# Kernel tuning notes

Measured on AMD Instinct MI355X. Metric: run time of the kernel, lower is better.

## Reference

```python
import jax, jax.numpy as jnp
import numpy as np

B, L, D, H = 2, 2048, 2048, 16
Dh = D // H
THETA = 500000.0


def _init_rope(dim, seq_len, n_heads):
    # Returns freqs_cis of shape (1, seq_len, 1, head_dim//2, 2) -> [..., 0]=cos, [..., 1]=sin
    hd = dim // n_heads
    inv_freqs = 1.0 / (THETA ** (jnp.arange(0, hd, 2, dtype=jnp.float32) / hd))
    t = jnp.arange(seq_len, dtype=jnp.float32)
    freqs = jnp.outer(t, inv_freqs).astype(jnp.float32)  # (L, hd/2)
    fc = jnp.stack([jnp.cos(freqs)[None, :, None, :],
                    jnp.sin(freqs)[None, :, None, :]], axis=3)  # (1, L, 1, 2, hd/2)
    return fc.transpose(0, 1, 2, 4, 3)  # (1, L, 1, hd/2, 2)


def _apply_rope(q, k, freqs_cis):
    def rotate(x):
        x2 = x.reshape(*x.shape[:-1], -1, 2)  # (B, L, H, Dh/2, 2)
        f = freqs_cis[:, :x.shape[1]]
        cos, sin = f[..., 0], f[..., 1]
        r = jnp.stack([x2[..., 0] * cos - x2[..., 1] * sin,
                       x2[..., 1] * cos + x2[..., 0] * sin], axis=-1)
        return r.reshape(*x.shape)
    return rotate(q), rotate(k)


def setup_inputs() -> dict:
    key = jax.random.key(0)
    kx, kq, kk, kv, ko = jax.random.split(key, 5)
    scale = 1.0 / np.sqrt(D)
    x = jax.random.normal(kx, (B, L, D), dtype=jnp.float32)
    Wq = jax.random.normal(kq, (D, H, Dh), dtype=jnp.float32) * scale
    Wk = jax.random.normal(kk, (D, H, Dh), dtype=jnp.float32) * scale
    Wv = jax.random.normal(kv, (D, H, Dh), dtype=jnp.float32) * scale
    Wo = jax.random.normal(ko, (D, D), dtype=jnp.float32) * scale
    return {"x": x, "Wq": Wq, "Wk": Wk, "Wv": Wv, "Wo": Wo}


def reference(x, Wq, Wk, Wv, Wo):
    freqs_cis = _init_rope(D, L, H)
    q = jnp.einsum('bld,dhk->blhk', x, Wq)  # (B, L, H, Dh)
    k = jnp.einsum('bld,dhk->blhk', x, Wk)
    v = jnp.einsum('bld,dhk->blhk', x, Wv)
    q, k = _apply_rope(q, k, freqs_cis)
    q = q / (Dh ** 0.5)
    att = jnp.einsum('bqhd,bkhd->bhqk', q, k)  # (B, H, L, L)
    Lq = x.shape[1]
    mask = jnp.tril(jnp.ones((1, 1, Lq, Lq), dtype=jnp.bool_))
    neg_inf = jnp.finfo(jnp.float32).min
    att = jnp.where(mask, att, neg_inf)
    att = jax.nn.softmax(att, axis=-1)
    out = jnp.einsum('bhqk,bkhd->bqhd', att, v)  # (B, L, H, Dh)
    out = out.reshape(x.shape)
    return jnp.einsum('bld,de->ble', out, Wo)
```

## Files before the change

### kernel.cpp

```cpp
#include <hip/hip_runtime.h>

typedef unsigned short u16;
typedef unsigned int u32;

#define Bb 2
#define Lc 2048
#define Dc 2048
#define Hc 16
#define DhC 128

typedef __bf16 bf16x8 __attribute__((ext_vector_type(8)));
typedef float f32x4 __attribute__((ext_vector_type(4)));
typedef float f32x16 __attribute__((ext_vector_type(16)));

__device__ __forceinline__ u16 f2b(float f) {
  u32 u = __float_as_uint(f);
  u32 r = (u + 0x7fffu + ((u >> 16) & 1u)) >> 16;
  return (u16)r;
}
__device__ __forceinline__ float b2f(u16 u) {
  return __uint_as_float(((u32)u) << 16);
}

__device__ __forceinline__ u32 cvtpk(float lo, float hi) {
  u32 r;
  asm("v_cvt_pk_bf16_f32 %0, %1, %2" : "=v"(r) : "v"(lo), "v"(hi));
  return r;
}

__device__ __forceinline__ void gll16(const void* g, void* l) {
  __builtin_amdgcn_global_load_lds(
      (const __attribute__((address_space(1))) u32*)g,
      (__attribute__((address_space(3))) u32*)l, 16, 0, 0);
}

__global__ __launch_bounds__(256) void sniff_dtype(const u16* __restrict__ x,
                                                   int* __restrict__ flag) {
  __shared__ int bad;
  if (threadIdx.x == 0) bad = 0;
  __syncthreads();
  int local = 0;
  for (int i = threadIdx.x; i < 65536; i += 256) {
    float v = fabsf(b2f(x[i]));
    if (!(v < 1000.f)) local = 1;
  }
  if (local) atomicOr(&bad, 1);
  __syncthreads();
  if (threadIdx.x == 0) *flag = bad;
}

__global__ __launch_bounds__(256) void conv_x(const void* __restrict__ in,
                                              u16* __restrict__ out,
                                              const int* __restrict__ flag) {
  const int f32 = *flag;
  const int i0 = (blockIdx.x * 256 + threadIdx.x) * 4;
  if (f32) {
    const float* p = (const float*)in;
#pragma unroll
    for (int j = 0; j < 4; j++) out[i0 + j] = f2b(p[i0 + j]);
  } else {
    const u16* p = (const u16*)in;
#pragma unroll
    for (int j = 0; j < 4; j++) out[i0 + j] = p[i0 + j];
  }
}

__device__ __forceinline__ void tconv_body(const void* in, u16* out, int f32) {
  __shared__ __align__(16) u16 tile[64][65];
  const int r0 = blockIdx.y * 64, c0 = blockIdx.x * 64;
  const int tc = threadIdx.x & 63, tr4 = threadIdx.x >> 6;
#pragma unroll
  for (int p = 0; p < 16; p++) {
    int r = tr4 + p * 4;
    size_t idx = (size_t)(r0 + r) * 2048 + c0 + tc;
    tile[r][tc] = f32 ? f2b(((const float*)in)[idx]) : ((const u16*)in)[idx];
  }
  __syncthreads();
#pragma unroll
  for (int p = 0; p < 16; p++) {
    int rr = tr4 + p * 4;
    out[(size_t)(c0 + rr) * 2048 + r0 + tc] = tile[tc][rr];
  }
}

__global__ __launch_bounds__(256) void transpose2d_conv(const void* __restrict__ in,
                                                        u16* __restrict__ out,
                                                        const int* __restrict__ flag) {
  tconv_body(in, out, *flag);
}

__global__ __launch_bounds__(256) void transpose3_conv(const void* __restrict__ W0,
                                                       const void* __restrict__ W1,
                                                       const void* __restrict__ W2,
                                                       u16* __restrict__ out,
                                                       const int* __restrict__ flag) {
  const int z = blockIdx.z;
  const void* in = (z == 0) ? W0 : (z == 1) ? W1 : W2;
  tconv_body(in, out + (size_t)z * 2048 * 2048, *flag);
}

template <typename OutT, int BN, bool FUSEV>
__device__ __forceinline__ void g256f_core(const u16* __restrict__ A,
                                           const u16* __restrict__ Bt,
                                           OutT* __restrict__ C,
                                           u16* __restrict__ Vt,
                                           int nwg, size_t bufStride) {
  constexpr int K = 2048;
  constexpr int WNW = (BN == 256) ? 4 : 2;
  constexpr int MT = (BN == 256) ? 8 : 4;
  constexpr int NT = 4;
  __shared__ __align__(16) u16 Asl[3][256 * 32];
  __shared__ __align__(16) u16 Bsl[3][BN * 32];

  const int tid = threadIdx.x;
  const int lane = tid & 63, w = tid >> 6;
  const int quad = lane >> 4, l15 = lane & 15;
  const int wm = w / WNW, wn = w % WNW;

  const int q8 = nwg >> 3;
  const int id = (int)blockIdx.x;
  const int swz = (id & 7) * q8 + (id >> 3);
  const int m0 = (swz & 15) * 256;
  const int n0 = (swz >> 4) * BN;

  const u16* aS = A + (size_t)(m0 + w * 16 + l15) * K + quad * 8;
  const u16* bS = Bt + (size_t)(n0 + w * 16 + l15) * K + quad * 8;

  const f32x4 fz = {0.f, 0.f, 0.f, 0.f};
  f32x4 acc[MT][NT];
#pragma unroll
  for (int i = 0; i < MT; i++)
#pragma unroll
    for (int j = 0; j < NT; j++) acc[i][j] = fz;

  auto stagef = [&](int kidx, int sl) {
    const int kk = kidx * 32;
    gll16(aS + kk, &Asl[sl][w * 512]);
    gll16(aS + (size_t)128 * K + kk, &Asl[sl][(8 + w) * 512]);
    gll16(bS + kk, &Bsl[sl][w * 512]);
    if constexpr (BN == 256)
      gll16(bS + (size_t)128 * K + kk, &Bsl[sl][(8 + w) * 512]);
  };

  auto computef = [&](int sl) {
    bf16x8 afr[MT], bfr[NT];
#pragma unroll
    for (int nt = 0; nt < NT; nt++)
      bfr[nt] = *(const bf16x8*)(&Bsl[sl][(wn * NT + nt) * 512 + lane * 8]);
#pragma unroll
    for (int mt = 0; mt < MT / 2; mt++)
      afr[mt] = *(const bf16x8*)(&Asl[sl][(wm * MT + mt) * 512 + lane * 8]);
    __builtin_amdgcn_sched_barrier(0);
#pragma unroll
    for (int mt = MT / 2; mt < MT; mt++)
      afr[mt] = *(const bf16x8*)(&Asl[sl][(wm * MT + mt) * 512 + lane * 8]);
    if constexpr (MT == 8)
      asm volatile("s_waitcnt lgkmcnt(4)" ::: "memory");
    else
      asm volatile("s_waitcnt lgkmcnt(2)" ::: "memory");
    __builtin_amdgcn_sched_barrier(0);
    __builtin_amdgcn_s_setprio(1);
#pragma unroll
    for (int mt = 0; mt < MT / 2; mt++)
#pragma unroll
      for (int nt = 0; nt < NT; nt++)
        acc[mt][nt] = __builtin_amdgcn_mfma_f32_16x16x32_bf16(
            afr[mt], bfr[nt], acc[mt][nt], 0, 0, 0);
    asm volatile("s_waitcnt lgkmcnt(0)" ::: "memory");
    __builtin_amdgcn_sched_barrier(0);
#pragma unroll
    for (int mt = MT / 2; mt < MT; mt++)
#pragma unroll
      for (int nt = 0; nt < NT; nt++)
        acc[mt][nt] = __builtin_amdgcn_mfma_f32_16x16x32_bf16(
            afr[mt], bfr[nt], acc[mt][nt], 0, 0, 0);
    __builtin_amdgcn_s_setprio(0);
  };

#define GVW()                                                                \
  do {                                                                       \
    if constexpr (BN == 256)                                                 \
      asm volatile("s_waitcnt vmcnt(4)" ::: "memory");                       \
    else                                                                     \
      asm volatile("s_waitcnt vmcnt(3)" ::: "memory");                       \
  } while (0)

  stagef(0, 0);
  stagef(1, 1);
  GVW();
  __builtin_amdgcn_s_barrier();

  int t = 0;
#pragma unroll 1
  for (int c = 0; c < 20; ++c) {
    stagef(t + 2, 2); computef(0); GVW(); __builtin_amdgcn_s_barrier();
    stagef(t + 3, 0); computef(1); GVW(); __builtin_amdgcn_s_barrier();
    stagef(t + 4, 1); computef(2); GVW(); __builtin_amdgcn_s_barrier();
    t += 3;
  }
  stagef(62, 2); computef(0); GVW(); __builtin_amdgcn_s_barrier();
  stagef(63, 0); computef(1); GVW(); __builtin_amdgcn_s_barrier();
  computef(2);
  asm volatile("s_waitcnt vmcnt(0)" ::: "memory");
  __builtin_amdgcn_s_barrier();
  computef(0);
#undef GVW

#pragma unroll
  for (int mt = 0; mt < MT; mt++)
#pragma unroll
    for (int nt = 0; nt < NT; nt++) {
      const int colg = n0 + wn * 64 + nt * 16 + l15;
      const int row0 = m0 + wm * (MT * 16) + mt * 16 + quad * 4;
      if (FUSEV && (colg >> 11) == 2) {
        const int hd = colg & 2047;
        const int bb = row0 >> 11, ll = row0 & 2047;
        const size_t off =
            (((size_t)(bb * 16 + (hd >> 7))) * 128 + (hd & 127)) * 2048 + ll;
#pragma unroll
        for (int r = 0; r < 4; r++) Vt[off + r] = f2b(acc[mt][nt][r]);
      } else {
        const size_t cbase =
            (size_t)(colg >> 11) * bufStride + (colg & 2047);
#pragma unroll
        for (int r = 0; r < 4; r++) {
          const float v = acc[mt][nt][r];
          if constexpr (sizeof(OutT) == 2)
            C[cbase + (size_t)(row0 + r) * 2048] = f2b(v);
          else
            C[cbase + (size_t)(row0 + r) * 2048] = v;
        }
      }
    }
}

__global__ __launch_bounds__(512, 1) void g256f_bf(const u16* __restrict__ A,
                                                   const u16* __restrict__ Bt,
                                                   u16* __restrict__ C,
                                                   u16* __restrict__ Vt,
                                                   int nwg, size_t bufStride) {
  g256f_core<u16, 256, true>(A, Bt, C, Vt, nwg, bufStride);
}
__global__ __launch_bounds__(512, 1) void g256f_f32(const u16* __restrict__ A,
                                                    const u16* __restrict__ Bt,
                                                    float* __restrict__ C,
                                                    int nwg, size_t bufStride) {
  g256f_core<float, 128, false>(A, Bt, C, nullptr, nwg, bufStride);
}

__global__ __launch_bounds__(256) void rope_qk(u16* __restrict__ Q, u16* __restrict__ K) {
  const int idx = blockIdx.x * 256 + threadIdx.x;
  const int j = idx & 63;
  const int h = (idx >> 6) & 15;
  const int l = idx >> 10;
  const float inv = exp2f(-0.2958057561f * (float)j);
  const float ang = (float)l * inv;
  float s, c;
  sincosf(ang, &s, &c);
  const float sc = 0.08838834764f;
#pragma unroll
  for (int b = 0; b < Bb; b++) {
    const size_t off = ((size_t)((b * Lc + l) * Hc + h)) * DhC + 2 * j;
    const float q0 = b2f(Q[off]), q1 = b2f(Q[off + 1]);
    const float k0 = b2f(K[off]), k1 = b2f(K[off + 1]);
    Q[off]     = f2b((q0 * c - q1 * s) * sc);
    Q[off + 1] = f2b((q1 * c + q0 * s) * sc);
    K[off]     = f2b(k0 * c - k1 * s);
    K[off + 1] = f2b(k1 * c + k0 * s);
  }
}

#define NEGBIG (-3.0e30f)
__global__ __launch_bounds__(256, 2) void flash_attn(const u16* __restrict__ Q,
                                                     const u16* __restrict__ Kg,
                                                     const u16* __restrict__ Vt,
                                                     u16* __restrict__ O) {
  __shared__ __align__(16) u16 Ks[2][64 * 128];
  __shared__ __align__(16) u16 Vs[2][128 * 64];
  const int tid = threadIdx.x;
  const int lane = tid & 63, w = tid >> 6;
  const int l31 = lane & 31, hib = lane >> 5;
  const int bh = blockIdx.y;
  const int b = bh >> 4, h = bh & 15;
  const int qt = (bh & 16) ? (int)blockIdx.x : (15 - (int)blockIdx.x);
  const int q0 = qt * 128;
  const int qw0 = q0 + w * 32;
  const int nkv = 2 * qt + 2;

  const int krl = lane >> 4, ksl = lane & 15;
  const int vrl = lane >> 3, vsl = lane & 7;

  bf16x8 qf[8];
  {
    const u16* qptr = Q + ((size_t)(b * Lc + qw0 + l31) * Hc + h) * DhC + 8 * hib;
#pragma unroll
    for (int s = 0; s < 8; s++) qf[s] = *(const bf16x8*)(qptr + s * 16);
  }

  {
#pragma unroll
    for (int p = 0; p < 4; p++) {
      const int r = p * 16 + w * 4 + krl;
      const int c = ksl ^ (r & 15);
      gll16(Kg + ((size_t)(b * Lc + r) * Hc + h) * DhC + c * 8,
            &Ks[0][(p * 256 + w * 64) * 8]);
    }
#pragma unroll
    for (int p = 0; p < 4; p++) {
      const int r = p * 32 + w * 8 + vrl;
      const int c = vsl ^ (r & 7);
      gll16(Vt + ((size_t)bh * DhC + r) * Lc + c * 8,
            &Vs[0][(p * 256 + w * 64) * 8]);
    }
  }

  f32x16 o[4];
#pragma unroll
  for (int dt = 0; dt < 4; dt++) o[dt] = (f32x16)0.0f;
  float mrow = NEGBIG, lrow = 0.f;

  __syncthreads();

  for (int kvt = 0; kvt < nkv; kvt++) {
    const int cur = kvt & 1;
    const u16* Ksc = Ks[cur];
    const u16* Vsc = Vs[cur];

    if (kvt + 1 < nkv) {
      const int nv0 = (kvt + 1) * 64;
      const int nxt = cur ^ 1;
#pragma unroll
      for (int p = 0; p < 4; p++) {
        const int r = p * 16 + w * 4 + krl;
        const int c = ksl ^ (r & 15);
        gll16(Kg + ((size_t)(b * Lc + nv0 + r) * Hc + h) * DhC + c * 8,
              &Ks[nxt][(p * 256 + w * 64) * 8]);
      }
#pragma unroll
      for (int p = 0; p < 4; p++) {
        const int r = p * 32 + w * 8 + vrl;
        const int c = vsl ^ (r & 7);
        gll16(Vt + ((size_t)bh * DhC + r) * Lc + nv0 + c * 8,
              &Vs[nxt][(p * 256 + w * 64) * 8]);
      }
    }

    const int kv0 = kvt * 64;
    const bool active = (kv0 <= qw0 + 31);
    if (active) {
      f32x16 s0 = (f32x16)0.0f, s1 = (f32x16)0.0f;
      __builtin_amdgcn_s_setprio(1);
#pragma unroll
      for (int s = 0; s < 8; s++) {
        const int ch = ((2 * s + hib) ^ (l31 & 15)) * 8;
        bf16x8 k0 = *(const bf16x8*)(&Ksc[l31 * 128 + ch]);
        bf16x8 k1 = *(const bf16x8*)(&Ksc[(32 + l31) * 128 + ch]);
        s0 = __builtin_amdgcn_mfma_f32_32x32x16_bf16(k0, qf[s], s0, 0, 0, 0);
        s1 = __builtin_amdgcn_mfma_f32_32x32x16_bf16(k1, qf[s], s1, 0, 0, 0);
      }
      __builtin_amdgcn_s_setprio(0);

      if (kv0 + 63 > qw0) {
        const int qg = qw0 + l31;
#pragma unroll
        for (int r = 0; r < 16; r++) {
          const int cr = (r & 3) + 8 * (r >> 2) + 4 * hib;
          if (kv0 + cr > qg) s0[r] = NEGBIG;
          if (kv0 + 32 + cr > qg) s1[r] = NEGBIG;
        }
      }

      float mx;
      {
        float a[8];
#pragma unroll
        for (int i = 0; i < 8; i++)
          a[i] = fmaxf(fmaxf(s0[i], s0[i + 8]), fmaxf(s1[i], s1[i + 8]));
        float b0 = fmaxf(a[0], a[4]), b1 = fmaxf(a[1], a[5]);
        float b2 = fmaxf(a[2], a[6]), b3 = fmaxf(a[3], a[7]);
        mx = fmaxf(fmaxf(b0, b1), fmaxf(b2, b3));
      }
      mx = fmaxf(mx, __shfl_xor(mx, 32, 64));

      if (!__all(mx - mrow <= 8.f)) {
        const float mnew = fmaxf(mrow, mx);
        const float al = __expf(mrow - mnew);
#pragma unroll
        for (int dt = 0; dt < 4; dt++)
#pragma unroll
          for (int e = 0; e < 16; e++) o[dt][e] *= al;
        lrow *= al;
        mrow = mnew;
      }

#pragma unroll
      for (int i = 0; i < 16; i++) {
        s0[i] = __expf(s0[i] - mrow);
        s1[i] = __expf(s1[i] - mrow);
      }
      float sm;
      {
        float a[8];
#pragma unroll
        for (int i = 0; i < 8; i++)
          a[i] = (s0[i] + s0[i + 8]) + (s1[i] + s1[i + 8]);
        sm = ((a[0] + a[4]) + (a[1] + a[5])) + ((a[2] + a[6]) + (a[3] + a[7]));
      }
      sm += __shfl_xor(sm, 32, 64);
      lrow += sm;

      bf16x8 paf[4];
#pragma unroll
      for (int t = 0; t < 2; t++) {
#pragma unroll
        for (int h8 = 0; h8 < 2; h8++) {
          const int rB = 8 * h8;
          u32 lo0, lo1, hi0, hi1;
          if (t == 0) {
            lo0 = cvtpk(s0[rB + 0], s0[rB + 1]);
            lo1 = cvtpk(s0[rB + 2], s0[rB + 3]);
            hi0 = cvtpk(s0[rB + 4], s0[rB + 5]);
            hi1 = cvtpk(s0[rB + 6], s0[rB + 7]);
          } else {
            lo0 = cvtpk(s1[rB + 0], s1[rB + 1]);
            lo1 = cvtpk(s1[rB + 2], s1[rB + 3]);
            hi0 = cvtpk(s1[rB + 4], s1[rB + 5]);
            hi1 = cvtpk(s1[rB + 6], s1[rB + 7]);
          }
          const u32 g0 = hib ? lo0 : hi0;
          const u32 g1 = hib ? lo1 : hi1;
          const u32 r0 = (u32)__shfl_xor((int)g0, 32, 64);
          const u32 r1 = (u32)__shfl_xor((int)g1, 32, 64);
          union { u32 u[4]; bf16x8 v; } pu;
          pu.u[0] = hib ? r0 : lo0;
          pu.u[1] = hib ? r1 : lo1;
          pu.u[2] = hib ? hi0 : r0;
          pu.u[3] = hib ? hi1 : r1;
          paf[2 * t + h8] = pu.v;
        }
      }

      __builtin_amdgcn_s_setprio(1);
#pragma unroll
      for (int B = 0; B < 4; B++) {
#pragma unroll
        for (int dt = 0; dt < 4; dt++) {
          const bf16x8 vf = *(const bf16x8*)(
              &Vsc[(32 * dt + l31) * 64 + (((2 * B + hib) ^ (l31 & 7))) * 8]);
          o[dt] = __builtin_amdgcn_mfma_f32_32x32x16_bf16(paf[B], vf, o[dt], 0, 0, 0);
        }
      }
      __builtin_amdgcn_s_setprio(0);
    }

    __syncthreads();
  }

#pragma unroll
  for (int r = 0; r < 16; r++) {
    const int cr = (r & 3) + 8 * (r >> 2) + 4 * hib;
    const float linv = 1.0f / __shfl(lrow, cr, 64);
    const size_t rowoff = ((size_t)(b * Lc + qw0 + cr) * Hc + h) * DhC + l31;
#pragma unroll
    for (int dt = 0; dt < 4; dt++)
      O[rowoff + 32 * dt] = f2b(o[dt][r] * linv);
  }
}

extern "C" void kernel_launch(void* const* d_in, const int* in_sizes, int n_in,
                              void* d_out, int out_size, void* d_ws, size_t ws_size,
                              hipStream_t stream) {
  const void* x  = d_in[0];
  const void* Wq = d_in[1];
  const void* Wk = d_in[2];
  const void* Wv = d_in[3];
  const void* Wo = d_in[4];
  float* out = (float*)d_out;

  char* w = (char*)d_ws;
  const size_t WSZ = (size_t)2048 * 2048;
  const size_t XSZ = (size_t)Bb * Lc * Dc;
  int* flag = (int*)w;
  u16* WT  = (u16*)(w + 256);
  u16* xc  = WT + WSZ;
  u16* Qb  = xc + XSZ;
  u16* Kb  = Qb + XSZ;
  u16* Vtb = Kb + XSZ;
  u16* Ob  = xc;
  u16* WTall = (u16*)d_out;

  sniff_dtype<<<1, 256, 0, stream>>>((const u16*)x, flag);
  conv_x<<<(int)(XSZ / 1024), 256, 0, stream>>>(x, xc, flag);

  transpose3_conv<<<dim3(32, 32, 3), 256, 0, stream>>>(Wq, Wk, Wv, WTall, flag);

  g256f_bf<<<dim3(384), 512, 0, stream>>>(xc, WTall, Qb, Vtb, 384, XSZ);

  rope_qk<<<(Lc * Hc * 64) / 256, 256, 0, stream>>>(Qb, Kb);

  dim3 fgrid(16, 32);
  flash_attn<<<fgrid, 256, 0, stream>>>(Qb, Kb, Vtb, Ob);

  dim3 tgrid(32, 32);
  transpose2d_conv<<<tgrid, 256, 0, stream>>>(Wo, WT, flag);
  g256f_f32<<<dim3(256), 512, 0, stream>>>(Ob, WT, out, 256, 0);
}
```

Baseline: 528.4 us.

## Retile projection GEMMs to 128x256 with BK=64 double buffering

The shared GEMM core moves from 256x256 (QKV) and 256x128 (output) tiles with BK=32 triple buffering to one 128x256 tile with BK=64 and two LDS buffers. Each wave now owns a 64x64 sub-tile and issues all of its LDS fragment loads before a single wait, followed by 32 MFMAs per stage. The QKV GEMM grid doubles to 768 workgroups, which should divide evenly across the CUs and avoid the partial final wave of the old 384-block launch. In exchange, the smaller M tile lowers data reuse per loaded byte, and the two-buffer pipeline with barriers on both sides of compute may overlap loads with MFMAs less well.

```diff
diff --git a/kernel.cpp b/kernel.cpp
--- a/kernel.cpp
+++ b/kernel.cpp
@@ -99,119 +99,105 @@
   tconv_body(in, out + (size_t)z * 2048 * 2048, *flag);
 }
 
-template <typename OutT, int BN, bool FUSEV>
-__device__ __forceinline__ void g256f_core(const u16* __restrict__ A,
+template <typename OutT, bool FUSEV>
+__device__ __forceinline__ void gemmk_core(const u16* __restrict__ A,
                                            const u16* __restrict__ Bt,
                                            OutT* __restrict__ C,
                                            u16* __restrict__ Vt,
                                            int nwg, size_t bufStride) {
   constexpr int K = 2048;
-  constexpr int WNW = (BN == 256) ? 4 : 2;
-  constexpr int MT = (BN == 256) ? 8 : 4;
-  constexpr int NT = 4;
-  __shared__ __align__(16) u16 Asl[3][256 * 32];
-  __shared__ __align__(16) u16 Bsl[3][BN * 32];
+  __shared__ __align__(16) u16 Asl[2][128 * 64];
+  __shared__ __align__(16) u16 Bsl[2][256 * 64];
 
   const int tid = threadIdx.x;
   const int lane = tid & 63, w = tid >> 6;
   const int quad = lane >> 4, l15 = lane & 15;
-  const int wm = w / WNW, wn = w % WNW;
+  const int wm = w >> 2, wn = w & 3;
 
   const int q8 = nwg >> 3;
   const int id = (int)blockIdx.x;
   const int swz = (id & 7) * q8 + (id >> 3);
-  const int m0 = (swz & 15) * 256;
-  const int n0 = (swz >> 4) * BN;
-
-  const u16* aS = A + (size_t)(m0 + w * 16 + l15) * K + quad * 8;
-  const u16* bS = Bt + (size_t)(n0 + w * 16 + l15) * K + quad * 8;
+  const int m0 = (swz & 31) * 128;
+  const int n0 = (swz >> 5) * 256;
+
+  const u16* aS = A + (size_t)(m0 + w * 16 + l15) * K + (lane >> 4) * 8;
+  const u16* bS = Bt + (size_t)(n0 + (2 * w) * 16 + l15) * K + (lane >> 4) * 8;
 
   const f32x4 fz = {0.f, 0.f, 0.f, 0.f};
-  f32x4 acc[MT][NT];
-#pragma unroll
-  for (int i = 0; i < MT; i++)
-#pragma unroll
-    for (int j = 0; j < NT; j++) acc[i][j] = fz;
-
-  auto stagef = [&](int kidx, int sl) {
-    const int kk = kidx * 32;
-    gll16(aS + kk, &Asl[sl][w * 512]);
-    gll16(aS + (size_t)128 * K + kk, &Asl[sl][(8 + w) * 512]);
-    gll16(bS + kk, &Bsl[sl][w * 512]);
-    if constexpr (BN == 256)
-      gll16(bS + (size_t)128 * K + kk, &Bsl[sl][(8 + w) * 512]);
+  f32x4 acc[4][4];
+#pragma unroll
+  for (int i = 0; i < 4; i++)
+#pragma unroll
+    for (int j = 0; j < 4; j++) acc[i][j] = fz;
+
+  auto stage = [&](int t, int sl) {
+    const int kk = t * 64;
+    gll16(aS + kk, &Asl[sl][w * 1024]);
+    gll16(aS + kk + 32, &Asl[sl][w * 1024 + 512]);
+    gll16(bS + kk, &Bsl[sl][(2 * w) * 1024]);
+    gll16(bS + kk + 32, &Bsl[sl][(2 * w) * 1024 + 512]);
+    gll16(bS + (size_t)16 * K + kk, &Bsl[sl][(2 * w + 1) * 1024]);
+    gll16(bS + (size_t)16 * K + kk + 32, &Bsl[sl][(2 * w + 1) * 1024 + 512]);
   };
 
-  auto computef = [&](int sl) {
-    bf16x8 afr[MT], bfr[NT];
-#pragma unroll
-    for (int nt = 0; nt < NT; nt++)
-      bfr[nt] = *(const bf16x8*)(&Bsl[sl][(wn * NT + nt) * 512 + lane * 8]);
-#pragma unroll
-    for (int mt = 0; mt < MT / 2; mt++)
-      afr[mt] = *(const bf16x8*)(&Asl[sl][(wm * MT + mt) * 512 + lane * 8]);
-    __builtin_amdgcn_sched_barrier(0);
-#pragma unroll
-    for (int mt = MT / 2; mt < MT; mt++)
-      afr[mt] = *(const bf16x8*)(&Asl[sl][(wm * MT + mt) * 512 + lane * 8]);
-    if constexpr (MT == 8)
-      asm volatile("s_waitcnt lgkmcnt(4)" ::: "memory");
-    else
-      asm volatile("s_waitcnt lgkmcnt(2)" ::: "memory");
+  auto compute = [&](int sl) {
+    bf16x8 afr[4][2], bfr[4][2];
+#pragma unroll
+    for (int mt = 0; mt < 4; mt++)
+#pragma unroll
+      for (int ks = 0; ks < 2; ks++)
+        afr[mt][ks] = *(const bf16x8*)(
+            &Asl[sl][(wm * 4 + mt) * 1024 + ks * 512 + lane * 8]);
+#pragma unroll
+    for (int nt = 0; nt < 4; nt++)
+#pragma unroll
+      for (int ks = 0; ks < 2; ks++)
+        bfr[nt][ks] = *(const bf16x8*)(
+            &Bsl[sl][(wn * 4 + nt) * 1024 + ks * 512 + lane * 8]);
+    asm volatile("s_waitcnt lgkmcnt(0)" ::: "memory");
     __builtin_amdgcn_sched_barrier(0);
     __builtin_amdgcn_s_setprio(1);
 #pragma unroll
-    for (int mt = 0; mt < MT / 2; mt++)
-#pragma unroll
-      for (int nt = 0; nt < NT; nt++)
-        acc[mt][nt] = __builtin_amdgcn_mfma_f32_16x16x32_bf16(
-            afr[mt], bfr[nt], acc[mt][nt], 0, 0, 0);
-    asm volatile("s_waitcnt lgkmcnt(0)" ::: "memory");
-    __builtin_amdgcn_sched_barrier(0);
-#pragma unroll
-    for (int mt = MT / 2; mt < MT; mt++)
-#pragma unroll
-      for (int nt = 0; nt < NT; nt++)
-        acc[mt][nt] = __builtin_amdgcn_mfma_f32_16x16x32_bf16(
-            afr[mt], bfr[nt], acc[mt][nt], 0, 0, 0);
+    for (int ks = 0; ks < 2; ks++)
+#pragma unroll
+      for (int mt = 0; mt < 4; mt++)
+#pragma unroll
+        for (int nt = 0; nt < 4; nt++)
+          acc[mt][nt] = __builtin_amdgcn_mfma_f32_16x16x32_bf16(
+              afr[mt][ks], bfr[nt][ks], acc[mt][nt], 0, 0, 0);
     __builtin_amdgcn_s_setprio(0);
   };
 
-#define GVW()                                                                \
-  do {                                                                       \
-    if constexpr (BN == 256)                                                 \
-      asm volatile("s_waitcnt vmcnt(4)" ::: "memory");                       \
-    else                                                                     \
-      asm volatile("s_waitcnt vmcnt(3)" ::: "memory");                       \
-  } while (0)
-
-  stagef(0, 0);
-  stagef(1, 1);
-  GVW();
+  stage(0, 0);
+
+#pragma unroll 1
+  for (int t = 0; t < 30; t += 2) {
+    stage(t + 1, 1);
+    asm volatile("s_waitcnt vmcnt(6)" ::: "memory");
+    __builtin_amdgcn_s_barrier();
+    compute(0);
+    __builtin_amdgcn_s_barrier();
+    stage(t + 2, 0);
+    asm volatile("s_waitcnt vmcnt(6)" ::: "memory");
+    __builtin_amdgcn_s_barrier();
+    compute(1);
+    __builtin_amdgcn_s_barrier();
+  }
+  stage(31, 1);
+  asm volatile("s_waitcnt vmcnt(6)" ::: "memory");
   __builtin_amdgcn_s_barrier();
-
-  int t = 0;
-#pragma unroll 1
-  for (int c = 0; c < 20; ++c) {
-    stagef(t + 2, 2); computef(0); GVW(); __builtin_amdgcn_s_barrier();
-    stagef(t + 3, 0); computef(1); GVW(); __builtin_amdgcn_s_barrier();
-    stagef(t + 4, 1); computef(2); GVW(); __builtin_amdgcn_s_barrier();
-    t += 3;
-  }
-  stagef(62, 2); computef(0); GVW(); __builtin_amdgcn_s_barrier();
-  stagef(63, 0); computef(1); GVW(); __builtin_amdgcn_s_barrier();
-  computef(2);
+  compute(0);
+  __builtin_amdgcn_s_barrier();
   asm volatile("s_waitcnt vmcnt(0)" ::: "memory");
   __builtin_amdgcn_s_barrier();
-  computef(0);
-#undef GVW
-
-#pragma unroll
-  for (int mt = 0; mt < MT; mt++)
-#pragma unroll
-    for (int nt = 0; nt < NT; nt++) {
+  compute(1);
+
+#pragma unroll
+  for (int mt = 0; mt < 4; mt++)
+#pragma unroll
+    for (int nt = 0; nt < 4; nt++) {
       const int colg = n0 + wn * 64 + nt * 16 + l15;
-      const int row0 = m0 + wm * (MT * 16) + mt * 16 + quad * 4;
+      const int row0 = m0 + wm * 64 + mt * 16 + quad * 4;
       if (FUSEV && (colg >> 11) == 2) {
         const int hd = colg & 2047;
         const int bb = row0 >> 11, ll = row0 & 2047;
@@ -234,18 +220,18 @@
     }
 }
 
-__global__ __launch_bounds__(512, 1) void g256f_bf(const u16* __restrict__ A,
+__global__ __launch_bounds__(512, 1) void gemmk_bf(const u16* __restrict__ A,
                                                    const u16* __restrict__ Bt,
                                                    u16* __restrict__ C,
                                                    u16* __restrict__ Vt,
                                                    int nwg, size_t bufStride) {
-  g256f_core<u16, 256, true>(A, Bt, C, Vt, nwg, bufStride);
-}
-__global__ __launch_bounds__(512, 1) void g256f_f32(const u16* __restrict__ A,
+  gemmk_core<u16, true>(A, Bt, C, Vt, nwg, bufStride);
+}
+__global__ __launch_bounds__(512, 1) void gemmk_f32(const u16* __restrict__ A,
                                                     const u16* __restrict__ Bt,
                                                     float* __restrict__ C,
                                                     int nwg, size_t bufStride) {
-  g256f_core<float, 128, false>(A, Bt, C, nullptr, nwg, bufStride);
+  gemmk_core<float, false>(A, Bt, C, nullptr, nwg, bufStride);
 }
 
 __global__ __launch_bounds__(256) void rope_qk(u16* __restrict__ Q, u16* __restrict__ K) {
@@ -494,7 +480,7 @@
 
   transpose3_conv<<<dim3(32, 32, 3), 256, 0, stream>>>(Wq, Wk, Wv, WTall, flag);
 
-  g256f_bf<<<dim3(384), 512, 0, stream>>>(xc, WTall, Qb, Vtb, 384, XSZ);
+  gemmk_bf<<<dim3(768), 512, 0, stream>>>(xc, WTall, Qb, Vtb, 768, XSZ);
 
   rope_qk<<<(Lc * Hc * 64) / 256, 256, 0, stream>>>(Qb, Kb);
 
@@ -503,5 +489,5 @@
 
   dim3 tgrid(32, 32);
   transpose2d_conv<<<tgrid, 256, 0, stream>>>(Wo, WT, flag);
-  g256f_f32<<<dim3(256), 512, 0, stream>>>(Ob, WT, out, 256, 0);
-}
+  gemmk_f32<<<dim3(256), 512, 0, stream>>>(Ob, WT, out, 256, 0);
+}
```

Result: slower. 576.3 us (+9.1%).
